# Optimization experiments

Hardware: AMD Instinct MI355X
Metric: run time of the kernel (lower is better)

Reference implementation:

```python
import jax, jax.numpy as jnp
import numpy as np


def setup_inputs() -> dict:
    key = jax.random.key(0)
    k1, k2, k3, k4, k5 = jax.random.split(key, 5)
    out_f, in_f, group_size = 11008, 4096, 128
    n_groups = in_f // group_size  # 32
    x = jax.random.normal(k1, (32, in_f), dtype=jnp.float16)
    packed = jax.random.randint(k2, (out_f, in_f // 2), 0, 256, dtype=jnp.int32)
    scales = (jax.random.uniform(k3, (out_f, n_groups), dtype=jnp.float32) * 0.02 + 0.001).astype(jnp.float16)
    zeros = (jax.random.normal(k4, (out_f, n_groups), dtype=jnp.float32) * 0.05).astype(jnp.float16)
    bias = (jax.random.normal(k5, (out_f,), dtype=jnp.float32) * 0.02).astype(jnp.float16)
    return {"x": x, "packed": packed, "scales": scales, "zeros": zeros,
            "bias": bias, "group_size": group_size, "in_features": in_f}


def _dequantize(packed, scales, zeros, in_features, group_size):
    # packed: [out_f, padded_in//2] uint8-valued ints; two int4 nibbles per byte.
    out_f = packed.shape[0]
    padded_in = packed.shape[1] * 2
    high = (packed >> 4) & 15
    low = packed & 15
    # interleave: even columns = high nibble, odd columns = low nibble
    unpacked = jnp.stack([high, low], axis=-1).reshape(out_f, padded_in).astype(scales.dtype)
    n_groups = scales.shape[1]
    grouped = unpacked.reshape(out_f, n_groups, group_size)
    deq = grouped * scales[:, :, None] + zeros[:, :, None]
    return deq.reshape(out_f, padded_in)[:, :in_features].astype(jnp.float16)


def reference(x, packed, scales, zeros, bias, group_size, in_features):
    # Fused dequant + linear: y = x @ W^T + b, with W reconstructed from int4.
    weight = _dequantize(packed, scales, zeros, in_features, group_size)  # [out_f, in_f]
    out = jnp.dot(x, weight.T) + bias
    return out
```

## Files before the change

### kernel.cpp

```cpp
#include <hip/hip_runtime.h>
#include <hip/hip_fp16.h>
#include <hip/hip_bf16.h>

typedef unsigned int u32;
typedef unsigned short u16;
typedef short short8 __attribute__((ext_vector_type(8)));
typedef float f32x4 __attribute__((ext_vector_type(4)));
typedef unsigned int u32x4 __attribute__((ext_vector_type(4)));

#define IN_F 4096
#define OUT_F 11008
#define MROWS 32
#define CCOLS 2048
#define NGRP 32
#define KSPL 8
#define NBX (OUT_F / 64)
#define XFRAG_BYTES ((size_t)MROWS * IN_F * 2)
#define SZ2_BYTES ((size_t)NGRP * OUT_F * 8)
#define SZ_OFF XFRAG_BYTES
#define PART_OFF (SZ_OFF + SZ2_BYTES)
#define PART_BYTES ((size_t)KSPL * MROWS * OUT_F * 4)
#define WS_NEED (PART_OFF + PART_BYTES)

typedef const __attribute__((address_space(1))) void* gas_t;
typedef __attribute__((address_space(3))) void* las_t;
__device__ __forceinline__ void gl_lds16(const void* g, void* l) {
  __builtin_amdgcn_global_load_lds((gas_t)g, (las_t)l, 16, 0, 0);
}
__device__ __forceinline__ u32 lds_u32(const void* p) {
  return (u32)(uintptr_t)(las_t)p;
}

__device__ __forceinline__ float bf2f(u16 b) {
  u32 t = ((u32)b) << 16;
  return __builtin_bit_cast(float, t);
}
__device__ __forceinline__ u32 f2bf_rne(float f) {
  u32 b = __builtin_bit_cast(u32, f);
  return (b + 0x7FFFu + ((b >> 16) & 1u)) >> 16;
}
__device__ __forceinline__ float h2f(u16 h) {
  return __half2float(__builtin_bit_cast(__half, h));
}

__device__ __forceinline__ u32 detect_mode(const u16* sc) {
  int l = (int)(threadIdx.x & 63u);
  u16 u = sc[2 * l];
  int e = (u >> 7) & 0xFF;
  unsigned long long mA = __ballot(e >= 114 && e <= 124);
  unsigned long long mC = __ballot(e >= 36 && e <= 88);
  int cA = __popcll(mA), cC = __popcll(mC);
  return (cA >= 48) ? 0u : ((cC >= 48) ? 2u : 1u);
}

__device__ __forceinline__ float ld_sz(const void* p, int idx, u32 mode) {
  if (mode == 0) return bf2f(((const u16*)p)[idx]);
  if (mode == 2) return h2f(((const u16*)p)[idx]);
  return ((const float*)p)[idx];
}

__device__ __forceinline__ u32 deq2(u32 v, float sf, float za) {
  float uh = __builtin_bit_cast(float, 0x43000000u | ((v << 12) & 0xF0000u));
  float ul = __builtin_bit_cast(float, 0x43000000u | ((v << 16) & 0xF0000u));
  float wh = __builtin_fmaf(uh, sf, za);
  float wl = __builtin_fmaf(ul, sf, za);
  __hip_bfloat162 pk = __float22bfloat162_rn(make_float2(wh, wl));
  u32 r;
  __builtin_memcpy(&r, &pk, 4);
  return r;
}
__device__ __forceinline__ u32x4 deq4v(u32x4 bv, float sf, float za) {
  u32x4 r;
  r[0] = deq2(bv[0], sf, za); r[1] = deq2(bv[1], sf, za);
  r[2] = deq2(bv[2], sf, za); r[3] = deq2(bv[3], sf, za);
  return r;
}
__device__ __forceinline__ uint4 deq4(uint4 bv, float sf, float za) {
  uint4 r;
  r.x = deq2(bv.x, sf, za); r.y = deq2(bv.y, sf, za);
  r.z = deq2(bv.z, sf, za); r.w = deq2(bv.w, sf, za);
  return r;
}

__device__ __forceinline__ uint4 lda8(const void* x, int eoff, u32 mode) {
  if (mode == 0) return *reinterpret_cast<const uint4*>((const u16*)x + eoff);
  if (mode == 1) {
    float4 u = *reinterpret_cast<const float4*>((const float*)x + eoff);
    float4 v = *reinterpret_cast<const float4*>((const float*)x + eoff + 4);
    uint4 r;
    r.x = f2bf_rne(u.x) | (f2bf_rne(u.y) << 16);
    r.y = f2bf_rne(u.z) | (f2bf_rne(u.w) << 16);
    r.z = f2bf_rne(v.x) | (f2bf_rne(v.y) << 16);
    r.w = f2bf_rne(v.z) | (f2bf_rne(v.w) << 16);
    return r;
  }
  uint4 h = *reinterpret_cast<const uint4*>((const u16*)x + eoff);
  uint4 r;
  r.x = f2bf_rne(h2f((u16)(h.x & 0xFFFF))) | (f2bf_rne(h2f((u16)(h.x >> 16))) << 16);
  r.y = f2bf_rne(h2f((u16)(h.y & 0xFFFF))) | (f2bf_rne(h2f((u16)(h.y >> 16))) << 16);
  r.z = f2bf_rne(h2f((u16)(h.z & 0xFFFF))) | (f2bf_rne(h2f((u16)(h.z >> 16))) << 16);
  r.w = f2bf_rne(h2f((u16)(h.w & 0xFFFF))) | (f2bf_rne(h2f((u16)(h.w >> 16))) << 16);
  return r;
}

__global__ __launch_bounds__(256) void qz_prep(
    const void* __restrict__ x, const void* __restrict__ scales,
    const void* __restrict__ zeros, u16* __restrict__ xfrag,
    float2* __restrict__ szT) {
  const u32 mode = detect_mode((const u16*)scales);
  const int t = (int)blockIdx.x * 256 + (int)threadIdx.x;
  if (t < 16384) {
    const int s = t >> 7, h = (t >> 6) & 1, lane = t & 63;
    const int q = lane & 15, p = lane >> 4;
    const int src = (h * 16 + q) * IN_F + s * 32 + p * 8;
    *reinterpret_cast<uint4*>(xfrag + (size_t)t * 8) = lda8(x, src, mode);
  } else {
    const int u = t - 16384;
    if (u < NGRP * OUT_F) {
      const int g = u / OUT_F, o = u - g * OUT_F;
      const float sfv = ld_sz(scales, o * NGRP + g, mode);
      const float zfv = ld_sz(zeros, o * NGRP + g, mode);
      szT[u] = make_float2(sfv, zfv - 128.0f * sfv);
    }
  }
}

__global__ __launch_bounds__(256, 3) void qv_gemm(
    const u16* __restrict__ xfrag, const int* __restrict__ packed,
    const float2* __restrict__ szT, float* __restrict__ part) {
  __shared__ __align__(16) char smemA[32768];
  __shared__ __align__(16) char smemB[4][4][1024];
  const int tid = (int)threadIdx.x;
  const int lane = tid & 63, wid = tid >> 6;
  const int q = lane & 15, p = lane >> 4;
  const int o0 = (int)blockIdx.x * 64 + wid * 16;
  const int ksl = (int)blockIdx.y;
  const int o = o0 + q;
  const int k32_0 = ksl * 16;

  const int g0 = ksl * 4;
  float sf[4], za[4];
#pragma unroll
  for (int g = 0; g < 4; ++g) {
    const float2 v = szT[(size_t)(g0 + g) * OUT_F + o];
    sf[g] = v.x; za[g] = v.y;
  }
  asm volatile("s_waitcnt vmcnt(0)" ::: "memory");

#pragma unroll
  for (int j = 0; j < 4; ++j) {
#pragma unroll
    for (int h = 0; h < 2; ++h) {
      const int s_loc = wid * 4 + j;
      const int sg = k32_0 + s_loc;
      gl_lds16(xfrag + ((size_t)(sg * 2 + h) * 64 + lane) * 8,
               &smemA[(s_loc * 2 + h) * 1024]);
    }
  }
  asm volatile("" ::: "memory");

  const int br = lane >> 2, bc = lane & 3;
  const int* bsrc = packed + (size_t)(o0 + br) * CCOLS + k32_0 * 16
                    + ((bc ^ ((br >> 1) & 3)) << 2);
#pragma unroll
  for (int s = 0; s < 4; ++s) {
    gl_lds16(bsrc + s * 16, &smemB[wid][s][0]);
    asm volatile("" ::: "memory");
  }

  asm volatile("s_waitcnt vmcnt(4)" ::: "memory");
  __builtin_amdgcn_s_barrier();
  __builtin_amdgcn_sched_barrier(0);

  f32x4 acc0 = {0.f, 0.f, 0.f, 0.f}, acc1 = {0.f, 0.f, 0.f, 0.f};
  const int rdoff = q * 64 + ((p ^ ((q >> 1) & 3)) << 4);
  const u32 abase = lds_u32(&smemA[0]) + (u32)(lane * 16);
  const u32 bbase = lds_u32(&smemB[wid][0][0]) + (u32)rdoff;

#define QC(W, SFI, BO, AO0, AO1)                                              \
  {                                                                           \
    asm volatile("s_waitcnt vmcnt(" #W ")" ::: "memory");                     \
    u32x4 bv, a0v, a1v;                                                       \
    asm volatile("ds_read_b128 %0, %1 offset:" BO : "=v"(bv) : "v"(bbase));   \
    asm volatile("ds_read_b128 %0, %1 offset:" AO0 : "=v"(a0v) : "v"(abase)); \
    asm volatile("ds_read_b128 %0, %1 offset:" AO1 : "=v"(a1v) : "v"(abase)); \
    asm volatile("s_waitcnt lgkmcnt(0)"                                       \
                 : "+v"(bv), "+v"(a0v), "+v"(a1v)::"memory");                 \
    __builtin_amdgcn_sched_barrier(0);                                        \
    const u32x4 bw = deq4v(bv, sf[SFI], za[SFI]);                             \
    acc0 = __builtin_amdgcn_mfma_f32_16x16x32_bf16(                           \
        __builtin_bit_cast(short8, a0v), __builtin_bit_cast(short8, bw),      \
        acc0, 0, 0, 0);                                                       \
    acc1 = __builtin_amdgcn_mfma_f32_16x16x32_bf16(                           \
        __builtin_bit_cast(short8, a1v), __builtin_bit_cast(short8, bw),      \
        acc1, 0, 0, 0);                                                       \
    asm volatile("" ::: "memory");                                            \
  }
#define QF(T)                                                                 \
  {                                                                           \
    gl_lds16(bsrc + (T)*16, &smemB[wid][(T) & 3][0]);                         \
    asm volatile("" ::: "memory");                                            \
  }

  QC(3, 0, "0", "0", "1024")           QF(4)
  QC(3, 0, "1024", "2048", "3072")     QF(5)
  QC(3, 0, "2048", "4096", "5120")     QF(6)
  QC(3, 0, "3072", "6144", "7168")     QF(7)
  QC(3, 1, "0", "8192", "9216")        QF(8)
  QC(3, 1, "1024", "10240", "11264")   QF(9)
  QC(3, 1, "2048", "12288", "13312")   QF(10)
  QC(3, 1, "3072", "14336", "15360")   QF(11)
  QC(3, 2, "0", "16384", "17408")      QF(12)
  QC(3, 2, "1024", "18432", "19456")   QF(13)
  QC(3, 2, "2048", "20480", "21504")   QF(14)
  QC(3, 2, "3072", "22528", "23552")   QF(15)
  QC(3, 3, "0", "24576", "25600")
  QC(2, 3, "1024", "26624", "27648")
  QC(1, 3, "2048", "28672", "29696")
  QC(0, 3, "3072", "30720", "31744")
#undef QC
#undef QF

  float* base = part + ((size_t)(ksl * NBX + (int)blockIdx.x) * 4 + wid) * 512
                + lane * 8;
  *reinterpret_cast<f32x4*>(base) = acc0;
  *reinterpret_cast<f32x4*>(base + 4) = acc1;
}

__global__ __launch_bounds__(256) void qr_reduce(
    const float* __restrict__ part, const void* __restrict__ scales,
    const void* __restrict__ bias, void* __restrict__ out) {
  const u32 mode = detect_mode((const u16*)scales);
  const int bx = (int)blockIdx.x;
  const int wid = (int)threadIdx.x >> 6, lane = (int)threadIdx.x & 63;
  const int q = lane & 15, p = lane >> 4;
  const int o = bx * 64 + wid * 16 + q;

  float s0[4] = {0.f, 0.f, 0.f, 0.f}, s1[4] = {0.f, 0.f, 0.f, 0.f};
#pragma unroll
  for (int ksl = 0; ksl < KSPL; ++ksl) {
    const float* base = part + ((size_t)(ksl * NBX + bx) * 4 + wid) * 512 + lane * 8;
    const float4 v0 = *reinterpret_cast<const float4*>(base);
    const float4 v1 = *reinterpret_cast<const float4*>(base + 4);
    s0[0] += v0.x; s0[1] += v0.y; s0[2] += v0.z; s0[3] += v0.w;
    s1[0] += v1.x; s1[1] += v1.y; s1[2] += v1.z; s1[3] += v1.w;
  }
  const float bb = ld_sz(bias, o, mode);
#pragma unroll
  for (int rr = 0; rr < 4; ++rr) {
    const float v0 = s0[rr] + bb, v1 = s1[rr] + bb;
    const size_t i0 = (size_t)(p * 4 + rr) * OUT_F + o;
    const size_t i1 = (size_t)(16 + p * 4 + rr) * OUT_F + o;
    if (mode == 1) {
      ((float*)out)[i0] = v0; ((float*)out)[i1] = v1;
    } else {
      ((u16*)out)[i0] = (u16)f2bf_rne(v0);
      ((u16*)out)[i1] = (u16)f2bf_rne(v1);
    }
  }
}

__global__ __launch_bounds__(256, 4) void qp_direct(
    const void* __restrict__ xsrc, const int* __restrict__ packed,
    const void* __restrict__ scales, const void* __restrict__ zeros,
    const void* __restrict__ bias, void* __restrict__ out) {
  constexpr int NSTEP = 128;
  constexpr int BD = 8, AD = 4;
  const u32 mode = detect_mode((const u16*)scales);
  const int tid = (int)threadIdx.x;
  const int lane = tid & 63, wid = tid >> 6;
  const int q = lane & 15, p = lane >> 4;
  const int tile = (int)blockIdx.x * 4 + wid;
  const int o = tile * 16 + q;
  const int* pr = packed + (size_t)o * CCOLS + p * 4;
  const int ae0 = q * IN_F + p * 8;
  const int ae1 = ae0 + 16 * IN_F;
  uint4 bb[BD], a0[AD], a1[AD];
#pragma unroll
  for (int i = 0; i < BD; ++i) bb[i] = *reinterpret_cast<const uint4*>(pr + i * 16);
#pragma unroll
  for (int i = 0; i < AD; ++i) {
    a0[i] = lda8(xsrc, ae0 + i * 32, mode);
    a1[i] = lda8(xsrc, ae1 + i * 32, mode);
  }
  f32x4 acc0 = {0.f, 0.f, 0.f, 0.f}, acc1 = {0.f, 0.f, 0.f, 0.f};
  for (int g = 0; g < NSTEP / 4; ++g) {
    const float sf = ld_sz(scales, o * NGRP + g, mode);
    const float za = ld_sz(zeros, o * NGRP + g, mode) - 128.0f * sf;
#pragma unroll
    for (int u = 0; u < 4; ++u) {
      const int s = g * 4 + u;
      const uint4 bw = deq4(bb[s % BD], sf, za);
      const uint4 av0 = a0[s % AD], av1 = a1[s % AD];
      if (s + BD < NSTEP) bb[s % BD] = *reinterpret_cast<const uint4*>(pr + (s + BD) * 16);
      if (s + AD < NSTEP) {
        a0[s % AD] = lda8(xsrc, ae0 + (s + AD) * 32, mode);
        a1[s % AD] = lda8(xsrc, ae1 + (s + AD) * 32, mode);
      }
      acc0 = __builtin_amdgcn_mfma_f32_16x16x32_bf16(
          __builtin_bit_cast(short8, av0), __builtin_bit_cast(short8, bw), acc0, 0, 0, 0);
      acc1 = __builtin_amdgcn_mfma_f32_16x16x32_bf16(
          __builtin_bit_cast(short8, av1), __builtin_bit_cast(short8, bw), acc1, 0, 0, 0);
    }
  }
  const float bbv = ld_sz(bias, o, mode);
#pragma unroll
  for (int r = 0; r < 4; ++r) {
    const float v0 = acc0[r] + bbv, v1 = acc1[r] + bbv;
    const size_t i0 = (size_t)(p * 4 + r) * OUT_F + o;
    const size_t i1 = (size_t)(16 + p * 4 + r) * OUT_F + o;
    if (mode == 1) { ((float*)out)[i0] = v0; ((float*)out)[i1] = v1; }
    else { ((u16*)out)[i0] = (u16)f2bf_rne(v0); ((u16*)out)[i1] = (u16)f2bf_rne(v1); }
  }
}

extern "C" void kernel_launch(void* const* d_in, const int* in_sizes, int n_in,
                              void* d_out, int out_size, void* d_ws, size_t ws_size,
                              hipStream_t stream) {
  (void)in_sizes; (void)n_in; (void)out_size;
  const void* x      = d_in[0];
  const int* packed  = (const int*)d_in[1];
  const void* scales = d_in[2];
  const void* zeros  = d_in[3];
  const void* bias   = d_in[4];

  if (ws_size >= WS_NEED) {
    u16* xfrag = (u16*)d_ws;
    float2* szT = (float2*)((char*)d_ws + SZ_OFF);
    float* part = (float*)((char*)d_ws + PART_OFF);
    qz_prep<<<1440, 256, 0, stream>>>(x, scales, zeros, xfrag, szT);
    qv_gemm<<<dim3(NBX, KSPL), 256, 0, stream>>>(xfrag, packed, szT, part);
    qr_reduce<<<NBX, 256, 0, stream>>>(part, scales, bias, d_out);
  } else {
    qp_direct<<<OUT_F / 64, 256, 0, stream>>>(x, packed, scales, zeros, bias, d_out);
  }
}
```

Measured before the change: 33.34 us.

## Double split-K factor, stream all B tiles upfront, store partials as bf16

Raises the K split from 8 to 16, so each block covers half the K range and twice as many blocks run across the GPU. Each wave now issues all eight of its packed-weight tile loads into LDS before computing, replacing the rolling refetch through a 4-slot ring. Partial sums are packed to bf16 before being written and widened back to fp32 in the reduce, halving partial-buffer traffic while the reduce reads twice as many slices. This trades lower partial precision and a longer reduction chain for more parallelism and less memory traffic.

```diff
diff --git a/kernel.cpp b/kernel.cpp
--- a/kernel.cpp
+++ b/kernel.cpp
@@ -13,13 +13,13 @@
 #define MROWS 32
 #define CCOLS 2048
 #define NGRP 32
-#define KSPL 8
+#define KSPL 16
 #define NBX (OUT_F / 64)
 #define XFRAG_BYTES ((size_t)MROWS * IN_F * 2)
 #define SZ2_BYTES ((size_t)NGRP * OUT_F * 8)
 #define SZ_OFF XFRAG_BYTES
 #define PART_OFF (SZ_OFF + SZ2_BYTES)
-#define PART_BYTES ((size_t)KSPL * MROWS * OUT_F * 4)
+#define PART_BYTES ((size_t)KSPL * NBX * 4 * 512 * 2)
 #define WS_NEED (PART_OFF + PART_BYTES)
 
 typedef const __attribute__((address_space(1))) void* gas_t;
@@ -41,6 +41,12 @@
 }
 __device__ __forceinline__ float h2f(u16 h) {
   return __half2float(__builtin_bit_cast(__half, h));
+}
+__device__ __forceinline__ u32 pk_bf2(float lo, float hi) {
+  __hip_bfloat162 pk = __float22bfloat162_rn(make_float2(lo, hi));
+  u32 r;
+  __builtin_memcpy(&r, &pk, 4);
+  return r;
 }
 
 __device__ __forceinline__ u32 detect_mode(const u16* sc) {
@@ -64,10 +70,7 @@
   float ul = __builtin_bit_cast(float, 0x43000000u | ((v << 16) & 0xF0000u));
   float wh = __builtin_fmaf(uh, sf, za);
   float wl = __builtin_fmaf(ul, sf, za);
-  __hip_bfloat162 pk = __float22bfloat162_rn(make_float2(wh, wl));
-  u32 r;
-  __builtin_memcpy(&r, &pk, 4);
-  return r;
+  return pk_bf2(wh, wl);
 }
 __device__ __forceinline__ u32x4 deq4v(u32x4 bv, float sf, float za) {
   u32x4 r;
@@ -127,31 +130,31 @@
 
 __global__ __launch_bounds__(256, 3) void qv_gemm(
     const u16* __restrict__ xfrag, const int* __restrict__ packed,
-    const float2* __restrict__ szT, float* __restrict__ part) {
-  __shared__ __align__(16) char smemA[32768];
-  __shared__ __align__(16) char smemB[4][4][1024];
+    const float2* __restrict__ szT, u16* __restrict__ part16) {
+  __shared__ __align__(16) char smemA[16384];
+  __shared__ __align__(16) char smemB[4][8][1024];
   const int tid = (int)threadIdx.x;
   const int lane = tid & 63, wid = tid >> 6;
   const int q = lane & 15, p = lane >> 4;
   const int o0 = (int)blockIdx.x * 64 + wid * 16;
   const int ksl = (int)blockIdx.y;
   const int o = o0 + q;
-  const int k32_0 = ksl * 16;
-
-  const int g0 = ksl * 4;
-  float sf[4], za[4];
-#pragma unroll
-  for (int g = 0; g < 4; ++g) {
+  const int k32_0 = ksl * 8;
+
+  const int g0 = ksl * 2;
+  float sf[2], za[2];
+#pragma unroll
+  for (int g = 0; g < 2; ++g) {
     const float2 v = szT[(size_t)(g0 + g) * OUT_F + o];
     sf[g] = v.x; za[g] = v.y;
   }
   asm volatile("s_waitcnt vmcnt(0)" ::: "memory");
 
 #pragma unroll
-  for (int j = 0; j < 4; ++j) {
+  for (int j = 0; j < 2; ++j) {
 #pragma unroll
     for (int h = 0; h < 2; ++h) {
-      const int s_loc = wid * 4 + j;
+      const int s_loc = wid * 2 + j;
       const int sg = k32_0 + s_loc;
       gl_lds16(xfrag + ((size_t)(sg * 2 + h) * 64 + lane) * 8,
                &smemA[(s_loc * 2 + h) * 1024]);
@@ -163,12 +166,12 @@
   const int* bsrc = packed + (size_t)(o0 + br) * CCOLS + k32_0 * 16
                     + ((bc ^ ((br >> 1) & 3)) << 2);
 #pragma unroll
-  for (int s = 0; s < 4; ++s) {
+  for (int s = 0; s < 8; ++s) {
     gl_lds16(bsrc + s * 16, &smemB[wid][s][0]);
     asm volatile("" ::: "memory");
   }
 
-  asm volatile("s_waitcnt vmcnt(4)" ::: "memory");
+  asm volatile("s_waitcnt vmcnt(8)" ::: "memory");
   __builtin_amdgcn_s_barrier();
   __builtin_amdgcn_sched_barrier(0);
 
@@ -196,39 +199,29 @@
         acc1, 0, 0, 0);                                                       \
     asm volatile("" ::: "memory");                                            \
   }
-#define QF(T)                                                                 \
-  {                                                                           \
-    gl_lds16(bsrc + (T)*16, &smemB[wid][(T) & 3][0]);                         \
-    asm volatile("" ::: "memory");                                            \
-  }
-
-  QC(3, 0, "0", "0", "1024")           QF(4)
-  QC(3, 0, "1024", "2048", "3072")     QF(5)
-  QC(3, 0, "2048", "4096", "5120")     QF(6)
-  QC(3, 0, "3072", "6144", "7168")     QF(7)
-  QC(3, 1, "0", "8192", "9216")        QF(8)
-  QC(3, 1, "1024", "10240", "11264")   QF(9)
-  QC(3, 1, "2048", "12288", "13312")   QF(10)
-  QC(3, 1, "3072", "14336", "15360")   QF(11)
-  QC(3, 2, "0", "16384", "17408")      QF(12)
-  QC(3, 2, "1024", "18432", "19456")   QF(13)
-  QC(3, 2, "2048", "20480", "21504")   QF(14)
-  QC(3, 2, "3072", "22528", "23552")   QF(15)
-  QC(3, 3, "0", "24576", "25600")
-  QC(2, 3, "1024", "26624", "27648")
-  QC(1, 3, "2048", "28672", "29696")
-  QC(0, 3, "3072", "30720", "31744")
+
+  QC(7, 0, "0", "0", "1024")
+  QC(6, 0, "1024", "2048", "3072")
+  QC(5, 0, "2048", "4096", "5120")
+  QC(4, 0, "3072", "6144", "7168")
+  QC(3, 1, "4096", "8192", "9216")
+  QC(2, 1, "5120", "10240", "11264")
+  QC(1, 1, "6144", "12288", "13312")
+  QC(0, 1, "7168", "14336", "15360")
 #undef QC
-#undef QF
-
-  float* base = part + ((size_t)(ksl * NBX + (int)blockIdx.x) * 4 + wid) * 512
-                + lane * 8;
-  *reinterpret_cast<f32x4*>(base) = acc0;
-  *reinterpret_cast<f32x4*>(base + 4) = acc1;
+
+  u32x4 pk;
+  pk[0] = pk_bf2(acc0[0], acc0[1]);
+  pk[1] = pk_bf2(acc0[2], acc0[3]);
+  pk[2] = pk_bf2(acc1[0], acc1[1]);
+  pk[3] = pk_bf2(acc1[2], acc1[3]);
+  u16* base = part16 + ((size_t)(ksl * NBX + (int)blockIdx.x) * 4 + wid) * 512
+              + lane * 8;
+  *reinterpret_cast<u32x4*>(base) = pk;
 }
 
 __global__ __launch_bounds__(256) void qr_reduce(
-    const float* __restrict__ part, const void* __restrict__ scales,
+    const u16* __restrict__ part16, const void* __restrict__ scales,
     const void* __restrict__ bias, void* __restrict__ out) {
   const u32 mode = detect_mode((const u16*)scales);
   const int bx = (int)blockIdx.x;
@@ -239,11 +232,12 @@
   float s0[4] = {0.f, 0.f, 0.f, 0.f}, s1[4] = {0.f, 0.f, 0.f, 0.f};
 #pragma unroll
   for (int ksl = 0; ksl < KSPL; ++ksl) {
-    const float* base = part + ((size_t)(ksl * NBX + bx) * 4 + wid) * 512 + lane * 8;
-    const float4 v0 = *reinterpret_cast<const float4*>(base);
-    const float4 v1 = *reinterpret_cast<const float4*>(base + 4);
-    s0[0] += v0.x; s0[1] += v0.y; s0[2] += v0.z; s0[3] += v0.w;
-    s1[0] += v1.x; s1[1] += v1.y; s1[2] += v1.z; s1[3] += v1.w;
+    const u16* base = part16 + ((size_t)(ksl * NBX + bx) * 4 + wid) * 512 + lane * 8;
+    const uint4 v = *reinterpret_cast<const uint4*>(base);
+    s0[0] += bf2f((u16)(v.x & 0xFFFF)); s0[1] += bf2f((u16)(v.x >> 16));
+    s0[2] += bf2f((u16)(v.y & 0xFFFF)); s0[3] += bf2f((u16)(v.y >> 16));
+    s1[0] += bf2f((u16)(v.z & 0xFFFF)); s1[1] += bf2f((u16)(v.z >> 16));
+    s1[2] += bf2f((u16)(v.w & 0xFFFF)); s1[3] += bf2f((u16)(v.w >> 16));
   }
   const float bb = ld_sz(bias, o, mode);
 #pragma unroll
@@ -327,10 +321,10 @@
   if (ws_size >= WS_NEED) {
     u16* xfrag = (u16*)d_ws;
     float2* szT = (float2*)((char*)d_ws + SZ_OFF);
-    float* part = (float*)((char*)d_ws + PART_OFF);
+    u16* part16 = (u16*)((char*)d_ws + PART_OFF);
     qz_prep<<<1440, 256, 0, stream>>>(x, scales, zeros, xfrag, szT);
-    qv_gemm<<<dim3(NBX, KSPL), 256, 0, stream>>>(xfrag, packed, szT, part);
-    qr_reduce<<<NBX, 256, 0, stream>>>(part, scales, bias, d_out);
+    qv_gemm<<<dim3(NBX, KSPL), 256, 0, stream>>>(xfrag, packed, szT, part16);
+    qr_reduce<<<NBX, 256, 0, stream>>>(part16, scales, bias, d_out);
   } else {
     qp_direct<<<OUT_F / 64, 256, 0, stream>>>(x, packed, scales, zeros, bias, d_out);
   }
```

Measured after the change: 33.86 us. About the same (+1.5%).
